# Kernel tuning notes

Hardware: AMD Instinct MI355X
Metric: run time of the kernel (lower is better)

Reference implementation:

```python
import jax, jax.numpy as jnp
import numpy as np


def setup_inputs() -> dict:
    key = jax.random.key(0)
    k1, k2, k3, k4 = jax.random.split(key, 4)
    N, F, E = 131072, 512, 256
    x = jax.random.normal(k1, (N, F), dtype=jnp.float32)
    W = jax.random.normal(k2, (E, F), dtype=jnp.float32) * 0.05  # stacked weak-classifier weights
    b = jax.random.normal(k3, (E,), dtype=jnp.float32) * 0.05
    alphas = jax.random.normal(k4, (E,), dtype=jnp.float32)
    return {"x": x, "W": W, "b": b, "alphas": alphas}


def reference(x, W, b, alphas):
    # Fused version of the per-estimator Python loop:
    # per estimator e: pred_e = round(sigmoid(x @ W[e] + b[e])) in {0,1}
    logits = jnp.einsum('nf,ef->ne', x, W) + b              # [N, E]
    preds = jnp.round(jax.nn.sigmoid(logits))               # [N, E], half-to-even like torch.round
    # original casts each (alpha * pred) term to long (trunc toward zero) before accumulating
    terms = jnp.trunc(alphas[None, :] * preds)              # [N, E]
    acc = jnp.sum(terms, axis=1)                            # [N]
    return jnp.sign(acc)
```

## Files before the change

### kernel.cpp

```cpp
#include <hip/hip_runtime.h>
#include <math.h>


#define F_DIM 512
#define BM    128
#define BK    32
#define NTMAX 8
#define KPAD  40
#define TAU   1e-3f

typedef float f32x4  __attribute__((ext_vector_type(4)));
typedef short bf16x8 __attribute__((ext_vector_type(8)));
typedef unsigned short u16x4 __attribute__((ext_vector_type(4)));

__device__ inline unsigned short bf16_rne(float v) {
    unsigned u = __float_as_uint(v);
    u += 0x7FFFu + ((u >> 16) & 1u);
    return (unsigned short)(u >> 16);
}
__device__ inline float bf16_to_f32(unsigned short h) {
    return __uint_as_float(((unsigned)h) << 16);
}

__device__ __attribute__((noinline)) bool exact_pred(const float* __restrict__ xr,
                                                     const float* __restrict__ wr,
                                                     float bv) {
    double s0 = 0.0, s1 = 0.0, s2 = 0.0, s3 = 0.0;
    for (int k = 0; k < F_DIM; k += 4) {
        s0 = fma((double)xr[k + 0], (double)wr[k + 0], s0);
        s1 = fma((double)xr[k + 1], (double)wr[k + 1], s1);
        s2 = fma((double)xr[k + 2], (double)wr[k + 2], s2);
        s3 = fma((double)xr[k + 3], (double)wr[k + 3], s3);
    }
    double s = ((s0 + s1) + (s2 + s3)) + (double)bv;
    return s > 0.0;
}

__global__ __launch_bounds__(256, 3)
void ada_mfma(const float* __restrict__ x, const float* __restrict__ W,
              const float* __restrict__ bias, const float* __restrict__ alphas,
              float* __restrict__ out) {
    __shared__ unsigned short xs_hi[BM][KPAD], xs_lo[BM][KPAD];
    __shared__ unsigned short wh[128][KPAD],  wl[128][KPAD];
    __shared__ int   se[272];
    __shared__ float st[272];
    __shared__ float sb[272];
    __shared__ int   wcnt[4];

    const int tid = threadIdx.x;
    const int n0  = blockIdx.x * BM;

    se[tid] = 0; st[tid] = 0.0f; sb[tid] = 0.0f;
    if (tid < 16) { se[256 + tid] = 0; st[256 + tid] = 0.0f; sb[256 + tid] = 0.0f; }
    __syncthreads();
    const float t = truncf(alphas[tid]);
    const bool flag = (t != 0.0f);
    const unsigned long long m64 = __ballot(flag);
    const int lane = tid & 63, wvi = tid >> 6;
    if (lane == 0) wcnt[wvi] = __popcll(m64);
    __syncthreads();
    int off = 0;
    #pragma unroll
    for (int w = 0; w < 4; ++w) if (w < wvi) off += wcnt[w];
    const int M = wcnt[0] + wcnt[1] + wcnt[2] + wcnt[3];
    if (flag) {
        const int slot = off + __popcll(m64 & ((1ull << lane) - 1ull));
        se[slot] = tid; st[slot] = t; sb[slot] = bias[tid];
    }
    __syncthreads();

    const int sr   = tid >> 3;
    const int sc   = (tid & 7) * 4;
    const int quad = (tid >> 4) & 3;
    const int l15  = tid & 15;
    const int rw   = (tid >> 6) * 32;

    const float* xp = x + (size_t)(n0 + sr) * F_DIM + sc;

    int part[2][4];
    #pragma unroll
    for (int mt = 0; mt < 2; ++mt)
        #pragma unroll
        for (int r = 0; r < 4; ++r) part[mt][r] = 0;

    for (int cb = 0; cb < M; cb += 128) {
        const int Mrem   = M - cb;
        const int NT     = (Mrem + 15) >> 4 < NTMAX ? (Mrem + 15) >> 4 : NTMAX;
        const int wstage = (NT + 1) >> 1;

        const float* wp[4];
        #pragma unroll
        for (int i = 0; i < 4; ++i) {
            const int e = se[cb + sr + i * 32];
            wp[i] = W + (size_t)e * F_DIM + sc;
        }

        f32x4 acc[2][NTMAX];
        #pragma unroll
        for (int mt = 0; mt < 2; ++mt)
            #pragma unroll
            for (int nt = 0; nt < NTMAX; ++nt)
                acc[mt][nt] = (f32x4){0.0f, 0.0f, 0.0f, 0.0f};

        for (int k0 = 0; k0 < F_DIM; k0 += BK) {
            float4 xv[4], wvv[4];
            #pragma unroll
            for (int i = 0; i < 4; ++i)
                xv[i] = *(const float4*)(xp + (size_t)i * 32 * F_DIM + k0);
            #pragma unroll
            for (int i = 0; i < 4; ++i)
                if (i < wstage) wvv[i] = *(const float4*)(wp[i] + k0);

            __syncthreads();

            #pragma unroll
            for (int i = 0; i < 4; ++i) {
                const int r = sr + i * 32;
                const float vv[4] = {xv[i].x, xv[i].y, xv[i].z, xv[i].w};
                u16x4 hv, lv;
                #pragma unroll
                for (int j = 0; j < 4; ++j) {
                    const unsigned short h = bf16_rne(vv[j]);
                    hv[j] = h;
                    lv[j] = bf16_rne(vv[j] - bf16_to_f32(h));
                }
                *(u16x4*)&xs_hi[r][sc] = hv;
                *(u16x4*)&xs_lo[r][sc] = lv;
            }
            #pragma unroll
            for (int i = 0; i < 4; ++i) {
                if (i < wstage) {
                    const int r = sr + i * 32;
                    const float vv[4] = {wvv[i].x, wvv[i].y, wvv[i].z, wvv[i].w};
                    u16x4 hv, lv;
                    #pragma unroll
                    for (int j = 0; j < 4; ++j) {
                        const unsigned short h = bf16_rne(vv[j]);
                        hv[j] = h;
                        lv[j] = bf16_rne(vv[j] - bf16_to_f32(h));
                    }
                    *(u16x4*)&wh[r][sc] = hv;
                    *(u16x4*)&wl[r][sc] = lv;
                }
            }

            __syncthreads();

            bf16x8 ah[2], al[2];
            #pragma unroll
            for (int mt = 0; mt < 2; ++mt) {
                ah[mt] = *(const bf16x8*)&xs_hi[rw + mt * 16 + l15][quad * 8];
                al[mt] = *(const bf16x8*)&xs_lo[rw + mt * 16 + l15][quad * 8];
            }
            #pragma unroll
            for (int nt = 0; nt < NTMAX; ++nt) {
                if (nt < NT) {
                    const bf16x8 bh = *(const bf16x8*)&wh[nt * 16 + l15][quad * 8];
                    const bf16x8 bl = *(const bf16x8*)&wl[nt * 16 + l15][quad * 8];
                    #pragma unroll
                    for (int mt = 0; mt < 2; ++mt) {
                        acc[mt][nt] = __builtin_amdgcn_mfma_f32_16x16x32_bf16(ah[mt], bh, acc[mt][nt], 0, 0, 0);
                        acc[mt][nt] = __builtin_amdgcn_mfma_f32_16x16x32_bf16(al[mt], bh, acc[mt][nt], 0, 0, 0);
                        acc[mt][nt] = __builtin_amdgcn_mfma_f32_16x16x32_bf16(ah[mt], bl, acc[mt][nt], 0, 0, 0);
                    }
                }
            }
        }

        #pragma unroll
        for (int nt = 0; nt < NTMAX; ++nt) {
            if (nt < NT) {
                const int col = cb + nt * 16 + l15;
                const float tv = st[col];
                if (tv != 0.0f) {
                    const float bv = sb[col];
                    const int it = (int)tv;
                    #pragma unroll
                    for (int mt = 0; mt < 2; ++mt) {
                        #pragma unroll
                        for (int r = 0; r < 4; ++r) {
                            const float logit = acc[mt][nt][r] + bv;
                            bool pred = (logit > 0.0f);
                            if (fabsf(logit) < TAU) {
                                const int row = rw + mt * 16 + quad * 4 + r;
                                pred = exact_pred(x + (size_t)(n0 + row) * F_DIM,
                                                  W + (size_t)se[col] * F_DIM, bv);
                            }
                            if (pred) part[mt][r] += it;
                        }
                    }
                }
            }
        }
    }

    #pragma unroll
    for (int mt = 0; mt < 2; ++mt) {
        #pragma unroll
        for (int r = 0; r < 4; ++r) {
            int v = part[mt][r];
            v += __shfl_xor(v, 1);
            v += __shfl_xor(v, 2);
            v += __shfl_xor(v, 4);
            v += __shfl_xor(v, 8);
            part[mt][r] = v;
        }
    }
    if (l15 == 0) {
        #pragma unroll
        for (int mt = 0; mt < 2; ++mt) {
            float4 o;
            o.x = (part[mt][0] > 0) ? 1.0f : (part[mt][0] < 0 ? -1.0f : 0.0f);
            o.y = (part[mt][1] > 0) ? 1.0f : (part[mt][1] < 0 ? -1.0f : 0.0f);
            o.z = (part[mt][2] > 0) ? 1.0f : (part[mt][2] < 0 ? -1.0f : 0.0f);
            o.w = (part[mt][3] > 0) ? 1.0f : (part[mt][3] < 0 ? -1.0f : 0.0f);
            *(float4*)(out + n0 + rw + mt * 16 + quad * 4) = o;
        }
    }
}

extern "C" void kernel_launch(void* const* d_in, const int* in_sizes, int n_in,
                              void* d_out, int out_size, void* d_ws, size_t ws_size,
                              hipStream_t stream) {
    const float* x      = (const float*)d_in[0];
    const float* W      = (const float*)d_in[1];
    const float* bias   = (const float*)d_in[2];
    const float* alphas = (const float*)d_in[3];
    float* out = (float*)d_out;

    const int n = in_sizes[0] / F_DIM;
    const int nblocks = n / BM;

    ada_mfma<<<dim3(nblocks), dim3(256), 0, stream>>>(x, W, bias, alphas, out);
}
```

Measured before the change: 493.6 us.

## Precompute split-bf16 weights in a prep kernel and drop LDS staging

Adds a small prep kernel that compacts the estimators with nonzero alpha and writes their weights as bf16 hi/lo pairs to workspace. The main kernel now loads x fragments straight from global memory into MFMA operand registers, converting in-register with a one-step register prefetch. Weight fragments are read directly from the precomputed global arrays, so all LDS staging and both per-tile barriers are gone. In exchange, x and W loads become strided 32-byte accesses per lane with no LDS reuse, and each block re-reads weights through cache, which adds global/L2 traffic and latency exposure.

```diff
diff --git a/kernel.cpp b/kernel.cpp
--- a/kernel.cpp
+++ b/kernel.cpp
@@ -2,12 +2,12 @@
 #include <math.h>
 
 
-#define F_DIM 512
-#define BM    128
-#define BK    32
-#define NTMAX 8
-#define KPAD  40
-#define TAU   1e-3f
+#define F_DIM  512
+#define BM     128
+#define BK     32
+#define NTMAX  8
+#define WSLOTS 256
+#define TAU    1e-3f
 
 typedef float f32x4  __attribute__((ext_vector_type(4)));
 typedef short bf16x8 __attribute__((ext_vector_type(8)));
@@ -20,6 +20,19 @@
 }
 __device__ inline float bf16_to_f32(unsigned short h) {
     return __uint_as_float(((unsigned)h) << 16);
+}
+
+__device__ inline void cvt8(const f32x4 a, const f32x4 b, bf16x8& hi, bf16x8& lo) {
+    #pragma unroll
+    for (int j = 0; j < 4; ++j) {
+        const float v0 = a[j], v1 = b[j];
+        const unsigned short h0 = bf16_rne(v0);
+        const unsigned short h1 = bf16_rne(v1);
+        hi[j]     = (short)h0;
+        hi[j + 4] = (short)h1;
+        lo[j]     = (short)bf16_rne(v0 - bf16_to_f32(h0));
+        lo[j + 4] = (short)bf16_rne(v1 - bf16_to_f32(h1));
+    }
 }
 
 __device__ __attribute__((noinline)) bool exact_pred(const float* __restrict__ xr,
@@ -36,22 +49,14 @@
     return s > 0.0;
 }
 
-__global__ __launch_bounds__(256, 3)
-void ada_mfma(const float* __restrict__ x, const float* __restrict__ W,
-              const float* __restrict__ bias, const float* __restrict__ alphas,
-              float* __restrict__ out) {
-    __shared__ unsigned short xs_hi[BM][KPAD], xs_lo[BM][KPAD];
-    __shared__ unsigned short wh[128][KPAD],  wl[128][KPAD];
-    __shared__ int   se[272];
-    __shared__ float st[272];
-    __shared__ float sb[272];
-    __shared__ int   wcnt[4];
-
+__global__ __launch_bounds__(256)
+void ada_prep(const float* __restrict__ W, const float* __restrict__ alphas,
+              unsigned short* __restrict__ whi, unsigned short* __restrict__ wlo) {
+    __shared__ int se[WSLOTS];
+    __shared__ int wcnt[4];
     const int tid = threadIdx.x;
-    const int n0  = blockIdx.x * BM;
-
-    se[tid] = 0; st[tid] = 0.0f; sb[tid] = 0.0f;
-    if (tid < 16) { se[256 + tid] = 0; st[256 + tid] = 0.0f; sb[256 + tid] = 0.0f; }
+
+    se[tid] = 0;
     __syncthreads();
     const float t = truncf(alphas[tid]);
     const bool flag = (t != 0.0f);
@@ -62,6 +67,50 @@
     int off = 0;
     #pragma unroll
     for (int w = 0; w < 4; ++w) if (w < wvi) off += wcnt[w];
+    if (flag) se[off + __popcll(m64 & ((1ull << lane) - 1ull))] = tid;
+    __syncthreads();
+
+    const int gstride = gridDim.x * blockDim.x;
+    for (int job = blockIdx.x * blockDim.x + tid; job < WSLOTS * (F_DIM / 4); job += gstride) {
+        const int col = job >> 7;
+        const int k4  = (job & 127) << 2;
+        const f32x4 v = *(const f32x4*)(W + (size_t)se[col] * F_DIM + k4);
+        u16x4 hv, lv;
+        #pragma unroll
+        for (int j = 0; j < 4; ++j) {
+            const unsigned short h = bf16_rne(v[j]);
+            hv[j] = h;
+            lv[j] = bf16_rne(v[j] - bf16_to_f32(h));
+        }
+        *(u16x4*)(whi + (size_t)col * F_DIM + k4) = hv;
+        *(u16x4*)(wlo + (size_t)col * F_DIM + k4) = lv;
+    }
+}
+
+__global__ __launch_bounds__(256, 3)
+void ada_mfma2(const float* __restrict__ x, const float* __restrict__ W,
+               const float* __restrict__ bias, const float* __restrict__ alphas,
+               const unsigned short* __restrict__ whi, const unsigned short* __restrict__ wlo,
+               float* __restrict__ out) {
+    __shared__ int   se[WSLOTS];
+    __shared__ float st[WSLOTS];
+    __shared__ float sb[WSLOTS];
+    __shared__ int   wcnt[4];
+
+    const int tid = threadIdx.x;
+    const int n0  = blockIdx.x * BM;
+
+    se[tid] = 0; st[tid] = 0.0f; sb[tid] = 0.0f;
+    __syncthreads();
+    const float t = truncf(alphas[tid]);
+    const bool flag = (t != 0.0f);
+    const unsigned long long m64 = __ballot(flag);
+    const int lane = tid & 63, wvi = tid >> 6;
+    if (lane == 0) wcnt[wvi] = __popcll(m64);
+    __syncthreads();
+    int off = 0;
+    #pragma unroll
+    for (int w = 0; w < 4; ++w) if (w < wvi) off += wcnt[w];
     const int M = wcnt[0] + wcnt[1] + wcnt[2] + wcnt[3];
     if (flag) {
         const int slot = off + __popcll(m64 & ((1ull << lane) - 1ull));
@@ -69,13 +118,12 @@
     }
     __syncthreads();
 
-    const int sr   = tid >> 3;
-    const int sc   = (tid & 7) * 4;
     const int quad = (tid >> 4) & 3;
     const int l15  = tid & 15;
     const int rw   = (tid >> 6) * 32;
 
-    const float* xp = x + (size_t)(n0 + sr) * F_DIM + sc;
+    const float* xp0 = x + (size_t)(n0 + rw + l15) * F_DIM + quad * 8;
+    const float* xp1 = xp0 + (size_t)16 * F_DIM;
 
     int part[2][4];
     #pragma unroll
@@ -84,16 +132,11 @@
         for (int r = 0; r < 4; ++r) part[mt][r] = 0;
 
     for (int cb = 0; cb < M; cb += 128) {
-        const int Mrem   = M - cb;
-        const int NT     = (Mrem + 15) >> 4 < NTMAX ? (Mrem + 15) >> 4 : NTMAX;
-        const int wstage = (NT + 1) >> 1;
-
-        const float* wp[4];
-        #pragma unroll
-        for (int i = 0; i < 4; ++i) {
-            const int e = se[cb + sr + i * 32];
-            wp[i] = W + (size_t)e * F_DIM + sc;
-        }
+        const int Mrem = M - cb;
+        const int NT   = (Mrem + 15) >> 4 < NTMAX ? (Mrem + 15) >> 4 : NTMAX;
+
+        const unsigned short* wph = whi + (size_t)(cb + l15) * F_DIM + quad * 8;
+        const unsigned short* wpl = wlo + (size_t)(cb + l15) * F_DIM + quad * 8;
 
         f32x4 acc[2][NTMAX];
         #pragma unroll
@@ -102,61 +145,29 @@
             for (int nt = 0; nt < NTMAX; ++nt)
                 acc[mt][nt] = (f32x4){0.0f, 0.0f, 0.0f, 0.0f};
 
+        f32x4 xv0 = *(const f32x4*)(xp0);
+        f32x4 xv1 = *(const f32x4*)(xp0 + 4);
+        f32x4 xv2 = *(const f32x4*)(xp1);
+        f32x4 xv3 = *(const f32x4*)(xp1 + 4);
+
         for (int k0 = 0; k0 < F_DIM; k0 += BK) {
-            float4 xv[4], wvv[4];
-            #pragma unroll
-            for (int i = 0; i < 4; ++i)
-                xv[i] = *(const float4*)(xp + (size_t)i * 32 * F_DIM + k0);
-            #pragma unroll
-            for (int i = 0; i < 4; ++i)
-                if (i < wstage) wvv[i] = *(const float4*)(wp[i] + k0);
-
-            __syncthreads();
-
-            #pragma unroll
-            for (int i = 0; i < 4; ++i) {
-                const int r = sr + i * 32;
-                const float vv[4] = {xv[i].x, xv[i].y, xv[i].z, xv[i].w};
-                u16x4 hv, lv;
-                #pragma unroll
-                for (int j = 0; j < 4; ++j) {
-                    const unsigned short h = bf16_rne(vv[j]);
-                    hv[j] = h;
-                    lv[j] = bf16_rne(vv[j] - bf16_to_f32(h));
-                }
-                *(u16x4*)&xs_hi[r][sc] = hv;
-                *(u16x4*)&xs_lo[r][sc] = lv;
+            bf16x8 ah[2], al[2];
+            cvt8(xv0, xv1, ah[0], al[0]);
+            cvt8(xv2, xv3, ah[1], al[1]);
+
+            const int kn = k0 + BK;
+            if (kn < F_DIM) {
+                xv0 = *(const f32x4*)(xp0 + kn);
+                xv1 = *(const f32x4*)(xp0 + kn + 4);
+                xv2 = *(const f32x4*)(xp1 + kn);
+                xv3 = *(const f32x4*)(xp1 + kn + 4);
             }
-            #pragma unroll
-            for (int i = 0; i < 4; ++i) {
-                if (i < wstage) {
-                    const int r = sr + i * 32;
-                    const float vv[4] = {wvv[i].x, wvv[i].y, wvv[i].z, wvv[i].w};
-                    u16x4 hv, lv;
-                    #pragma unroll
-                    for (int j = 0; j < 4; ++j) {
-                        const unsigned short h = bf16_rne(vv[j]);
-                        hv[j] = h;
-                        lv[j] = bf16_rne(vv[j] - bf16_to_f32(h));
-                    }
-                    *(u16x4*)&wh[r][sc] = hv;
-                    *(u16x4*)&wl[r][sc] = lv;
-                }
-            }
-
-            __syncthreads();
-
-            bf16x8 ah[2], al[2];
-            #pragma unroll
-            for (int mt = 0; mt < 2; ++mt) {
-                ah[mt] = *(const bf16x8*)&xs_hi[rw + mt * 16 + l15][quad * 8];
-                al[mt] = *(const bf16x8*)&xs_lo[rw + mt * 16 + l15][quad * 8];
-            }
+
             #pragma unroll
             for (int nt = 0; nt < NTMAX; ++nt) {
                 if (nt < NT) {
-                    const bf16x8 bh = *(const bf16x8*)&wh[nt * 16 + l15][quad * 8];
-                    const bf16x8 bl = *(const bf16x8*)&wl[nt * 16 + l15][quad * 8];
+                    const bf16x8 bh = *(const bf16x8*)(wph + (size_t)nt * 16 * F_DIM + k0);
+                    const bf16x8 bl = *(const bf16x8*)(wpl + (size_t)nt * 16 * F_DIM + k0);
                     #pragma unroll
                     for (int mt = 0; mt < 2; ++mt) {
                         acc[mt][nt] = __builtin_amdgcn_mfma_f32_16x16x32_bf16(ah[mt], bh, acc[mt][nt], 0, 0, 0);
@@ -231,5 +242,9 @@
     const int n = in_sizes[0] / F_DIM;
     const int nblocks = n / BM;
 
-    ada_mfma<<<dim3(nblocks), dim3(256), 0, stream>>>(x, W, bias, alphas, out);
-}
+    unsigned short* whi = (unsigned short*)d_ws;
+    unsigned short* wlo = whi + (size_t)WSLOTS * F_DIM;
+
+    ada_prep<<<dim3(64), dim3(256), 0, stream>>>(W, alphas, whi, wlo);
+    ada_mfma2<<<dim3(nblocks), dim3(256), 0, stream>>>(x, W, bias, alphas, whi, wlo, out);
+}
```

Result: slower. 535.5 us (+8.5%).
